# Kernel optimization log

Hardware: AMD Instinct MI355X
Metric: run time of the kernel (lower is better)

The kernel has to match this reference:

```python
import jax, jax.numpy as jnp
import numpy as np

B, N, I, O, H = 4, 2048, 256, 128, 8
THRESHOLD = 0.5
NEG = -1e10

def setup_inputs() -> dict:
    key = jax.random.key(0)
    ks = jax.random.split(key, 9)
    s = 0.05
    return {
        'h': jax.random.normal(ks[0], (B, N, I), dtype=jnp.float32),
        'adj': jax.random.uniform(ks[1], (B, N, N), dtype=jnp.float32),
        'conv_w': jax.random.normal(ks[2], (H, O, I), dtype=jnp.float32) * s,
        'conv_b': jax.random.normal(ks[3], (H, O), dtype=jnp.float32) * s,
        'a': jax.random.normal(ks[4], (H, 2 * O), dtype=jnp.float32) * s,
        'Wh1_bias': jax.random.normal(ks[5], (H, N, 1), dtype=jnp.float32) * s,
        'Wh2_bias': jax.random.normal(ks[6], (H, N, 1), dtype=jnp.float32) * s,
        'a_bias': jax.random.normal(ks[7], (H, N, N), dtype=jnp.float32) * s,
        'attention_bias': jax.random.normal(ks[8], (H, N, O), dtype=jnp.float32) * s,
    }

def reference(h, adj, conv_w, conv_b, a, Wh1_bias, Wh2_bias, a_bias, attention_bias):
    # Per-head 1x1 conv == per-head linear: (B,N,I) x (H,O,I) -> (B,H,N,O)
    Wh = jnp.einsum('bni,hoi->bhno', h, conv_w) + conv_b[None, :, None, :]
    a1 = a[:, :O]   # (H,O)
    a2 = a[:, O:]   # (H,O)
    Wh1 = jnp.einsum('bhno,ho->bhn', Wh, a1)[..., None] + Wh1_bias            # (B,H,N,1)
    # torch 'bhno,hol->bhln' transposes to (B,H,1,N); adding (H,N,1) bias broadcasts to (B,H,N,N)
    Wh2 = jnp.einsum('bhno,ho->bhn', Wh, a2)[:, :, None, :] + Wh2_bias[None]  # (B,H,N,N)
    e = jax.nn.leaky_relu(Wh1 + Wh2, negative_slope=0.2) + a_bias             # (B,H,N,N)
    scores = jnp.where(adj[:, None] >= THRESHOLD, e, NEG)
    att = jax.nn.softmax(scores, axis=3)                                      # (B,H,N,N)
    # torch.einsum('bhnn,bhno->bhno') takes the DIAGONAL of attention (repeated label)
    diag = jnp.diagonal(att, axis1=2, axis2=3)                                # (B,H,N)
    h_prime = jax.nn.elu(diag[..., None] * Wh + attention_bias)               # (B,H,N,O)
    return h_prime.transpose(0, 2, 1, 3).reshape(B, N, H * O)
```

## Files before the change

kernel.cpp:

```cpp
#include <hip/hip_runtime.h>

constexpr int B_ = 4, N_ = 2048, I_ = 256, O_ = 128, H_ = 8;
constexpr float LOG2E = 1.4426950408889634f;
constexpr int LDP = 132;
constexpr int GEMM_BLOCKS = 512;

#define EXP2(x) __builtin_amdgcn_exp2f(x)

__global__ __launch_bounds__(256) void gemm_mask(
    const float* __restrict__ hin, const float* __restrict__ cw,
    const float* __restrict__ cb, const float* __restrict__ a,
    const float* __restrict__ wb1, const float* __restrict__ wb2,
    const float* __restrict__ adj,
    float* __restrict__ Wh, float* __restrict__ u, float* __restrict__ v,
    unsigned char* __restrict__ nb)
{
  __shared__ float hsT[32 * LDP];
  __shared__ float wT[32 * LDP];
  const int tid = threadIdx.x;

  if (blockIdx.x >= GEMM_BLOCKS) {
    const int row = (blockIdx.x - GEMM_BLOCKS) * 4 + (tid >> 6);
    const int ml  = tid & 63;
    const float* arow = &adj[(size_t)row * N_];
    unsigned long long acc64 = 0ull;
    #pragma unroll
    for (int it = 0; it < 8; ++it) {
      int g = it * 64 + ml;
      float4 a4 = *(const float4*)&arow[g * 4];
      unsigned long long nib =
          (unsigned long long)(a4.x >= 0.5f)
        | ((unsigned long long)(a4.y >= 0.5f) << 1)
        | ((unsigned long long)(a4.z >= 0.5f) << 2)
        | ((unsigned long long)(a4.w >= 0.5f) << 3);
      acc64 |= nib << (8 * it);
    }
    *(unsigned long long*)&nb[(size_t)row * 512 + ml * 8] = acc64;
    return;
  }

  const int bid = blockIdx.x;
  const int n0  = (bid & 15) * 128;
  const int by  = bid >> 4;
  const int b   = by >> 3;
  const int hh  = by & 7;
  const int tn  = tid >> 4;
  const int to  = tid & 15;

  float acc[2][4][8];
  #pragma unroll
  for (int g = 0; g < 2; ++g)
    #pragma unroll
    for (int j = 0; j < 4; ++j)
      #pragma unroll
      for (int c = 0; c < 8; ++c) acc[g][j][c] = 0.f;

  for (int i0 = 0; i0 < I_; i0 += 32) {
    __syncthreads();
    #pragma unroll
    for (int kk = 0; kk < 4; ++kk) {
      int f4 = tid + kk * 256;
      int n  = f4 >> 3;
      int i4 = (f4 & 7) * 4;
      float4 hv = *(const float4*)&hin[((size_t)(b * N_ + n0 + n)) * I_ + i0 + i4];
      hsT[(i4 + 0) * LDP + n] = hv.x; hsT[(i4 + 1) * LDP + n] = hv.y;
      hsT[(i4 + 2) * LDP + n] = hv.z; hsT[(i4 + 3) * LDP + n] = hv.w;
      float4 wv = *(const float4*)&cw[((size_t)(hh * O_ + n)) * I_ + i0 + i4];
      wT[(i4 + 0) * LDP + n] = wv.x; wT[(i4 + 1) * LDP + n] = wv.y;
      wT[(i4 + 2) * LDP + n] = wv.z; wT[(i4 + 3) * LDP + n] = wv.w;
    }
    __syncthreads();
    #pragma unroll 8
    for (int k = 0; k < 32; ++k) {
      const float* hr = &hsT[k * LDP];
      const float* wr = &wT[k * LDP];
      float4 av0 = *(const float4*)&hr[tn * 4];
      float4 av1 = *(const float4*)&hr[64 + tn * 4];
      float4 bv0 = *(const float4*)&wr[to * 4];
      float4 bv1 = *(const float4*)&wr[64 + to * 4];
      float aj;
      #define FMA_ROW(G, J, COMP)                                         \
        aj = COMP;                                                        \
        acc[G][J][0] = fmaf(aj, bv0.x, acc[G][J][0]);                     \
        acc[G][J][1] = fmaf(aj, bv0.y, acc[G][J][1]);                     \
        acc[G][J][2] = fmaf(aj, bv0.z, acc[G][J][2]);                     \
        acc[G][J][3] = fmaf(aj, bv0.w, acc[G][J][3]);                     \
        acc[G][J][4] = fmaf(aj, bv1.x, acc[G][J][4]);                     \
        acc[G][J][5] = fmaf(aj, bv1.y, acc[G][J][5]);                     \
        acc[G][J][6] = fmaf(aj, bv1.z, acc[G][J][6]);                     \
        acc[G][J][7] = fmaf(aj, bv1.w, acc[G][J][7]);
      FMA_ROW(0, 0, av0.x) FMA_ROW(0, 1, av0.y) FMA_ROW(0, 2, av0.z) FMA_ROW(0, 3, av0.w)
      FMA_ROW(1, 0, av1.x) FMA_ROW(1, 1, av1.y) FMA_ROW(1, 2, av1.z) FMA_ROW(1, 3, av1.w)
      #undef FMA_ROW
    }
  }

  float4 cb0 = *(const float4*)&cb[hh * O_ + to * 4];
  float4 cb1 = *(const float4*)&cb[hh * O_ + to * 4 + 64];
  const float* ah = &a[hh * 2 * O_];
  float4 a1l = *(const float4*)&ah[to * 4];
  float4 a1h = *(const float4*)&ah[64 + to * 4];
  float4 a2l = *(const float4*)&ah[128 + to * 4];
  float4 a2h = *(const float4*)&ah[192 + to * 4];

  #pragma unroll
  for (int g = 0; g < 2; ++g) {
    #pragma unroll
    for (int j = 0; j < 4; ++j) {
      float* A = acc[g][j];
      A[0] += cb0.x; A[1] += cb0.y; A[2] += cb0.z; A[3] += cb0.w;
      A[4] += cb1.x; A[5] += cb1.y; A[6] += cb1.z; A[7] += cb1.w;
      int n = n0 + g * 64 + tn * 4 + j;
      size_t base = (((size_t)(b * N_ + n)) * H_ + hh) * O_;
      *(float4*)&Wh[base + to * 4]      = make_float4(A[0], A[1], A[2], A[3]);
      *(float4*)&Wh[base + to * 4 + 64] = make_float4(A[4], A[5], A[6], A[7]);

      float pu = A[0]*a1l.x + A[1]*a1l.y + A[2]*a1l.z + A[3]*a1l.w
               + A[4]*a1h.x + A[5]*a1h.y + A[6]*a1h.z + A[7]*a1h.w;
      float pv = A[0]*a2l.x + A[1]*a2l.y + A[2]*a2l.z + A[3]*a2l.w
               + A[4]*a2h.x + A[5]*a2h.y + A[6]*a2h.z + A[7]*a2h.w;
      #pragma unroll
      for (int off = 8; off; off >>= 1) {
        pu += __shfl_xor(pu, off);
        pv += __shfl_xor(pv, off);
      }
      if (to == 0) {
        int idx = (b * H_ + hh) * N_ + n;
        u[idx] = (pu + wb1[hh * N_ + n] + wb2[hh * N_ + n]) * LOG2E;
        v[idx] = pv * LOG2E;
      }
    }
  }
}

__global__ __launch_bounds__(256) void attn_fused(
    const unsigned char* __restrict__ nb, const float* __restrict__ abias,
    const float* __restrict__ u, const float* __restrict__ v,
    const float* __restrict__ Wh, const float* __restrict__ attb,
    float* __restrict__ out)
{
  const int r    = blockIdx.x;
  const int hh   = blockIdx.y;
  const int lane = threadIdx.x & 63;
  const int b    = threadIdx.x >> 6;
  const int bh   = b * H_ + hh;

  const float* vrow  = &v[(size_t)bh * N_];
  const float* abrow = &abias[((size_t)(hh * N_ + r)) * N_];
  const unsigned char* nrow = &nb[(size_t)(b * N_ + r) * 512];

  uint2 mk = *(const uint2*)&nrow[lane * 8];
  float4 vv[8], aa[8];
  #pragma unroll
  for (int kk = 0; kk < 8; ++kk) {
    int c4 = kk * 256 + lane * 4;
    vv[kk] = *(const float4*)&vrow[c4];
    aa[kk] = *(const float4*)&abrow[c4];
  }
  const size_t obase = (((size_t)(b * N_ + r)) * H_ + hh) * O_;
  const float* atr = &attb[((size_t)(hh * N_ + r)) * O_];
  float wh0 = Wh[obase + lane], wh1 = Wh[obase + lane + 64];
  float at0 = atr[lane],        at1 = atr[lane + 64];
  float uval = u[bh * N_ + r];
  float vdiag = vrow[r];

  float ss0 = 0.f, ss1 = 0.f, ss2 = 0.f, ss3 = 0.f;
  #pragma unroll
  for (int kk = 0; kk < 8; ++kk) {
    unsigned int nib =
        (kk < 4 ? (mk.x >> (kk * 8)) : (mk.y >> ((kk - 4) * 8))) & 0xffu;
    float4 v4 = vv[kk], a4 = aa[kk];
    float pre, lr, e;
    #define COL(J, VC, AC, SS)                                            \
      pre = uval + VC;                                                    \
      lr  = fmaxf(pre, 0.2f * pre);                                       \
      e   = EXP2(fmaf(AC, LOG2E, lr));                                    \
      SS += (nib & (1u << J)) ? e : 0.f;
    COL(0, v4.x, a4.x, ss0) COL(1, v4.y, a4.y, ss1)
    COL(2, v4.z, a4.z, ss2) COL(3, v4.w, a4.w, ss3)
    #undef COL
  }
  float ss = (ss0 + ss1) + (ss2 + ss3);
  #pragma unroll
  for (int off = 32; off; off >>= 1) ss += __shfl_xor(ss, off);

  int gd = r >> 2;
  unsigned int nibd = nrow[(gd & 63) * 8 + (gd >> 6)];
  float prd = uval + vdiag;
  float lrd = fmaxf(prd, 0.2f * prd);
  float numd = EXP2(fmaf(abrow[r], LOG2E, lrd));
  float diag = ((nibd >> (r & 3)) & 1u) ? numd / ss : 0.f;

  float x0 = fmaf(diag, wh0, at0);
  float x1 = fmaf(diag, wh1, at1);
  out[obase + lane]      = x0 > 0.f ? x0 : __expf(x0) - 1.f;
  out[obase + lane + 64] = x1 > 0.f ? x1 : __expf(x1) - 1.f;
}

extern "C" void kernel_launch(void* const* d_in, const int* in_sizes, int n_in,
                              void* d_out, int out_size, void* d_ws, size_t ws_size,
                              hipStream_t stream) {
  const float* hin   = (const float*)d_in[0];
  const float* adj   = (const float*)d_in[1];
  const float* cw    = (const float*)d_in[2];
  const float* cb    = (const float*)d_in[3];
  const float* a     = (const float*)d_in[4];
  const float* wb1   = (const float*)d_in[5];
  const float* wb2   = (const float*)d_in[6];
  const float* abias = (const float*)d_in[7];
  const float* attb  = (const float*)d_in[8];
  float* out = (float*)d_out;

  float* u = (float*)d_ws;
  float* v = u + (size_t)B_ * H_ * N_;
  unsigned char* nb = (unsigned char*)(v + (size_t)B_ * H_ * N_);
  float* whws = (float*)(nb + (size_t)B_ * N_ * 512);

  size_t needBytes = ((size_t)B_ * H_ * N_ * 2) * 4 + (size_t)B_ * N_ * 512
                   + (size_t)B_ * N_ * H_ * O_ * 4;
  float* Wh = (ws_size >= needBytes) ? whws : out;

  gemm_mask<<<dim3(GEMM_BLOCKS + B_ * N_ / 4), 256, 0, stream>>>(
      hin, cw, cb, a, wb1, wb2, adj, Wh, u, v, nb);
  attn_fused<<<dim3(N_, H_), 256, 0, stream>>>(nb, abias, u, v, Wh, attb, out);
}
```

Before: 352.6 us.

## Switch projection GEMM to bf16 MFMA with register-prefetched global loads

Replaces the fp32 FMA outer-product GEMM in gemm_mask with bf16 MFMA 16x16x32 instructions. Inputs are converted to bf16 when written to shared memory, and the next K-slice is prefetched into registers while the current one is computed. The epilogue is rewritten for the MFMA output layout, reducing u/v partials through shuffles and shared memory across two warps. This cuts GEMM compute time but lowers the precision of Wh, u and v to bf16-rounded inputs, and the Wh stores become scalar and less coalesced.

```diff
diff --git a/kernel.cpp b/kernel.cpp
--- a/kernel.cpp
+++ b/kernel.cpp
@@ -2,10 +2,18 @@
 
 constexpr int B_ = 4, N_ = 2048, I_ = 256, O_ = 128, H_ = 8;
 constexpr float LOG2E = 1.4426950408889634f;
-constexpr int LDP = 132;
 constexpr int GEMM_BLOCKS = 512;
 
+using bf16x8 = __attribute__((ext_vector_type(8))) short;
+using f32x4  = __attribute__((ext_vector_type(4))) float;
+
 #define EXP2(x) __builtin_amdgcn_exp2f(x)
+
+__device__ __forceinline__ unsigned pk_bf16(float lo, float hi) {
+  unsigned r;
+  asm("v_cvt_pk_bf16_f32 %0, %1, %2" : "=v"(r) : "v"(lo), "v"(hi));
+  return r;
+}
 
 __global__ __launch_bounds__(256) void gemm_mask(
     const float* __restrict__ hin, const float* __restrict__ cw,
@@ -15,8 +23,9 @@
     float* __restrict__ Wh, float* __restrict__ u, float* __restrict__ v,
     unsigned char* __restrict__ nb)
 {
-  __shared__ float hsT[32 * LDP];
-  __shared__ float wT[32 * LDP];
+  __shared__ __align__(16) short tA[128 * 40];
+  __shared__ __align__(16) short tB[128 * 40];
+  __shared__ float up[2][128], vp[2][128];
   const int tid = threadIdx.x;
 
   if (blockIdx.x >= GEMM_BLOCKS) {
@@ -44,92 +53,117 @@
   const int by  = bid >> 4;
   const int b   = by >> 3;
   const int hh  = by & 7;
-  const int tn  = tid >> 4;
-  const int to  = tid & 15;
-
-  float acc[2][4][8];
-  #pragma unroll
-  for (int g = 0; g < 2; ++g)
-    #pragma unroll
-    for (int j = 0; j < 4; ++j)
-      #pragma unroll
-      for (int c = 0; c < 8; ++c) acc[g][j][c] = 0.f;
-
-  for (int i0 = 0; i0 < I_; i0 += 32) {
+  const int lane = tid & 63, wid = tid >> 6;
+  const int wm = wid >> 1, wn = wid & 1;
+  const int lr = lane & 15;
+  const int lg = lane >> 4;
+
+  f32x4 acc[4][4];
+  #pragma unroll
+  for (int i = 0; i < 4; ++i)
+    #pragma unroll
+    for (int j = 0; j < 4; ++j) acc[i][j] = (f32x4){0.f, 0.f, 0.f, 0.f};
+
+  const int srow = tid >> 1;
+  const int skh  = (tid & 1) << 4;
+  const float* gA = &hin[((size_t)(b * N_ + n0 + srow)) * I_ + skh];
+  const float* gB = &cw[((size_t)(hh * O_ + srow)) * I_ + skh];
+  uint4* wA = (uint4*)&tA[srow * 40 + skh];
+  uint4* wB = (uint4*)&tB[srow * 40 + skh];
+
+  float4 ra[4], rb[4];
+  #pragma unroll
+  for (int q = 0; q < 4; ++q) {
+    ra[q] = *(const float4*)&gA[q * 4];
+    rb[q] = *(const float4*)&gB[q * 4];
+  }
+
+  for (int step = 0; step < 8; ++step) {
+    wA[0] = make_uint4(pk_bf16(ra[0].x, ra[0].y), pk_bf16(ra[0].z, ra[0].w),
+                       pk_bf16(ra[1].x, ra[1].y), pk_bf16(ra[1].z, ra[1].w));
+    wA[1] = make_uint4(pk_bf16(ra[2].x, ra[2].y), pk_bf16(ra[2].z, ra[2].w),
+                       pk_bf16(ra[3].x, ra[3].y), pk_bf16(ra[3].z, ra[3].w));
+    wB[0] = make_uint4(pk_bf16(rb[0].x, rb[0].y), pk_bf16(rb[0].z, rb[0].w),
+                       pk_bf16(rb[1].x, rb[1].y), pk_bf16(rb[1].z, rb[1].w));
+    wB[1] = make_uint4(pk_bf16(rb[2].x, rb[2].y), pk_bf16(rb[2].z, rb[2].w),
+                       pk_bf16(rb[3].x, rb[3].y), pk_bf16(rb[3].z, rb[3].w));
+    if (step < 7) {
+      int i0 = (step + 1) * 32;
+      #pragma unroll
+      for (int q = 0; q < 4; ++q) {
+        ra[q] = *(const float4*)&gA[i0 + q * 4];
+        rb[q] = *(const float4*)&gB[i0 + q * 4];
+      }
+    }
     __syncthreads();
-    #pragma unroll
-    for (int kk = 0; kk < 4; ++kk) {
-      int f4 = tid + kk * 256;
-      int n  = f4 >> 3;
-      int i4 = (f4 & 7) * 4;
-      float4 hv = *(const float4*)&hin[((size_t)(b * N_ + n0 + n)) * I_ + i0 + i4];
-      hsT[(i4 + 0) * LDP + n] = hv.x; hsT[(i4 + 1) * LDP + n] = hv.y;
-      hsT[(i4 + 2) * LDP + n] = hv.z; hsT[(i4 + 3) * LDP + n] = hv.w;
-      float4 wv = *(const float4*)&cw[((size_t)(hh * O_ + n)) * I_ + i0 + i4];
-      wT[(i4 + 0) * LDP + n] = wv.x; wT[(i4 + 1) * LDP + n] = wv.y;
-      wT[(i4 + 2) * LDP + n] = wv.z; wT[(i4 + 3) * LDP + n] = wv.w;
-    }
+    bf16x8 af[4], bf[4];
+    #pragma unroll
+    for (int im = 0; im < 4; ++im)
+      af[im] = *(const bf16x8*)&tA[(wm * 64 + im * 16 + lr) * 40 + lg * 8];
+    #pragma unroll
+    for (int in = 0; in < 4; ++in)
+      bf[in] = *(const bf16x8*)&tB[(wn * 64 + in * 16 + lr) * 40 + lg * 8];
+    #pragma unroll
+    for (int im = 0; im < 4; ++im)
+      #pragma unroll
+      for (int in = 0; in < 4; ++in)
+        acc[im][in] = __builtin_amdgcn_mfma_f32_16x16x32_bf16(
+            af[im], bf[in], acc[im][in], 0, 0, 0);
     __syncthreads();
-    #pragma unroll 8
-    for (int k = 0; k < 32; ++k) {
-      const float* hr = &hsT[k * LDP];
-      const float* wr = &wT[k * LDP];
-      float4 av0 = *(const float4*)&hr[tn * 4];
-      float4 av1 = *(const float4*)&hr[64 + tn * 4];
-      float4 bv0 = *(const float4*)&wr[to * 4];
-      float4 bv1 = *(const float4*)&wr[64 + to * 4];
-      float aj;
-      #define FMA_ROW(G, J, COMP)                                         \
-        aj = COMP;                                                        \
-        acc[G][J][0] = fmaf(aj, bv0.x, acc[G][J][0]);                     \
-        acc[G][J][1] = fmaf(aj, bv0.y, acc[G][J][1]);                     \
-        acc[G][J][2] = fmaf(aj, bv0.z, acc[G][J][2]);                     \
-        acc[G][J][3] = fmaf(aj, bv0.w, acc[G][J][3]);                     \
-        acc[G][J][4] = fmaf(aj, bv1.x, acc[G][J][4]);                     \
-        acc[G][J][5] = fmaf(aj, bv1.y, acc[G][J][5]);                     \
-        acc[G][J][6] = fmaf(aj, bv1.z, acc[G][J][6]);                     \
-        acc[G][J][7] = fmaf(aj, bv1.w, acc[G][J][7]);
-      FMA_ROW(0, 0, av0.x) FMA_ROW(0, 1, av0.y) FMA_ROW(0, 2, av0.z) FMA_ROW(0, 3, av0.w)
-      FMA_ROW(1, 0, av1.x) FMA_ROW(1, 1, av1.y) FMA_ROW(1, 2, av1.z) FMA_ROW(1, 3, av1.w)
-      #undef FMA_ROW
-    }
-  }
-
-  float4 cb0 = *(const float4*)&cb[hh * O_ + to * 4];
-  float4 cb1 = *(const float4*)&cb[hh * O_ + to * 4 + 64];
+  }
+
   const float* ah = &a[hh * 2 * O_];
-  float4 a1l = *(const float4*)&ah[to * 4];
-  float4 a1h = *(const float4*)&ah[64 + to * 4];
-  float4 a2l = *(const float4*)&ah[128 + to * 4];
-  float4 a2h = *(const float4*)&ah[192 + to * 4];
-
-  #pragma unroll
-  for (int g = 0; g < 2; ++g) {
-    #pragma unroll
-    for (int j = 0; j < 4; ++j) {
-      float* A = acc[g][j];
-      A[0] += cb0.x; A[1] += cb0.y; A[2] += cb0.z; A[3] += cb0.w;
-      A[4] += cb1.x; A[5] += cb1.y; A[6] += cb1.z; A[7] += cb1.w;
-      int n = n0 + g * 64 + tn * 4 + j;
-      size_t base = (((size_t)(b * N_ + n)) * H_ + hh) * O_;
-      *(float4*)&Wh[base + to * 4]      = make_float4(A[0], A[1], A[2], A[3]);
-      *(float4*)&Wh[base + to * 4 + 64] = make_float4(A[4], A[5], A[6], A[7]);
-
-      float pu = A[0]*a1l.x + A[1]*a1l.y + A[2]*a1l.z + A[3]*a1l.w
-               + A[4]*a1h.x + A[5]*a1h.y + A[6]*a1h.z + A[7]*a1h.w;
-      float pv = A[0]*a2l.x + A[1]*a2l.y + A[2]*a2l.z + A[3]*a2l.w
-               + A[4]*a2h.x + A[5]*a2h.y + A[6]*a2h.z + A[7]*a2h.w;
-      #pragma unroll
-      for (int off = 8; off; off >>= 1) {
-        pu += __shfl_xor(pu, off);
-        pv += __shfl_xor(pv, off);
-      }
-      if (to == 0) {
-        int idx = (b * H_ + hh) * N_ + n;
-        u[idx] = (pu + wb1[hh * N_ + n] + wb2[hh * N_ + n]) * LOG2E;
-        v[idx] = pv * LOG2E;
-      }
-    }
+  float a1v[4], a2v[4], cbv[4];
+  #pragma unroll
+  for (int in = 0; in < 4; ++in) {
+    int o = wn * 64 + in * 16 + lr;
+    a1v[in] = ah[o];
+    a2v[in] = ah[O_ + o];
+    cbv[in] = cb[hh * O_ + o];
+  }
+  #pragma unroll
+  for (int im = 0; im < 4; ++im) {
+    float su0 = 0.f, su1 = 0.f, su2 = 0.f, su3 = 0.f;
+    float sv0 = 0.f, sv1 = 0.f, sv2 = 0.f, sv3 = 0.f;
+    #pragma unroll
+    for (int in = 0; in < 4; ++in) {
+      int o = wn * 64 + in * 16 + lr;
+      #pragma unroll
+      for (int reg = 0; reg < 4; ++reg) {
+        float val = acc[im][in][reg] + cbv[in];
+        int n = n0 + wm * 64 + im * 16 + lg * 4 + reg;
+        Wh[(((size_t)(b * N_ + n)) * H_ + hh) * O_ + o] = val;
+        float s1 = fmaf(val, a1v[in], 0.f);
+        float s2 = fmaf(val, a2v[in], 0.f);
+        if (reg == 0) { su0 += s1; sv0 += s2; }
+        else if (reg == 1) { su1 += s1; sv1 += s2; }
+        else if (reg == 2) { su2 += s1; sv2 += s2; }
+        else { su3 += s1; sv3 += s2; }
+      }
+    }
+    float su[4] = {su0, su1, su2, su3};
+    float sv[4] = {sv0, sv1, sv2, sv3};
+    #pragma unroll
+    for (int reg = 0; reg < 4; ++reg) {
+      float x = su[reg], y = sv[reg];
+      #pragma unroll
+      for (int off = 1; off <= 8; off <<= 1) {
+        x += __shfl_xor(x, off);
+        y += __shfl_xor(y, off);
+      }
+      if (lr == 0) {
+        int tr = wm * 64 + im * 16 + lg * 4 + reg;
+        up[wn][tr] = x;
+        vp[wn][tr] = y;
+      }
+    }
+  }
+  __syncthreads();
+  if (tid < 128) {
+    int n = n0 + tid;
+    int idx = (b * H_ + hh) * N_ + n;
+    u[idx] = (up[0][tid] + up[1][tid] + wb1[hh * N_ + n] + wb2[hh * N_ + n]) * LOG2E;
+    v[idx] = (vp[0][tid] + vp[1][tid]) * LOG2E;
   }
 }
 
```

Result: faster. 311.8 us (-11.6%).
